# Kernel tuning notes

Measured on AMD Instinct MI355X. Metric: run time of the kernel, lower is better.

Reference implementation:

```python
import jax, jax.numpy as jnp
import numpy as np

N = 524288   # sparse points
C = 64       # io channels
AC = 128     # attn channels
H = 8        # heads
PS = 64      # patch size
HID = 256    # mlp hidden (mlp_ratio=2)
HD = AC // H # head dim
EPS = 1e-5


def _ln(x):
    mu = x.mean(-1, keepdims=True)
    v = x.var(-1, keepdims=True)
    return (x - mu) / jnp.sqrt(v + EPS)


def setup_inputs() -> dict:
    key = jax.random.key(0)
    ks = jax.random.split(key, 12)
    def w(k, shape, fan_in):
        return jax.random.normal(k, shape, jnp.float32) * (1.0 / np.sqrt(fan_in))
    return {
        "feats": jax.random.normal(ks[0], (N, C), jnp.float32),
        "w_pre": w(ks[1], (C, AC), C),    "b_pre": jnp.zeros((AC,), jnp.float32),
        "g1": jnp.ones((AC,), jnp.float32), "b1": jnp.zeros((AC,), jnp.float32),
        "w_qkv": w(ks[2], (AC, 3 * AC), AC), "b_qkv": jnp.zeros((3 * AC,), jnp.float32),
        "w_proj": w(ks[3], (AC, AC), AC), "b_proj": jnp.zeros((AC,), jnp.float32),
        "g2": jnp.ones((AC,), jnp.float32), "b2": jnp.zeros((AC,), jnp.float32),
        "w_m1": w(ks[4], (AC, HID), AC),  "b_m1": jnp.zeros((HID,), jnp.float32),
        "w_m2": w(ks[5], (HID, AC), HID), "b_m2": jnp.zeros((AC,), jnp.float32),
        "w_post": w(ks[6], (AC, C), AC),  "b_post": jnp.zeros((C,), jnp.float32),
    }


def reference(feats, w_pre, b_pre, g1, b1, w_qkv, b_qkv, w_proj, b_proj,
              g2, b2, w_m1, b_m1, w_m2, b_m2, w_post, b_post):
    # pre_proj: 1x1 sparse conv == pointwise linear on [N, C]
    x2 = feats @ w_pre + b_pre                            # [N, AC]
    # norm1 -> patch attention
    n1 = _ln(x2) * g1 + b1
    P = N // PS
    qkv = (n1 @ w_qkv + b_qkv).reshape(P, PS, 3, H, HD)   # patches of 64 pts
    q, k, v = qkv[:, :, 0], qkv[:, :, 1], qkv[:, :, 2]    # [P, PS, H, HD]
    scale = HD ** -0.5
    att = jnp.einsum('pqhd,pkhd->phqk', q, k) * scale     # [P, H, PS, PS]
    att = jax.nn.softmax(att, axis=-1)
    o = jnp.einsum('phqk,pkhd->pqhd', att, v).reshape(N, AC)
    h = o @ w_proj + b_proj
    x2 = x2 + h                                           # residual 1
    # norm2 -> pointwise MLP (1x1 conv -> GELU -> 1x1 conv)
    n2 = _ln(x2) * g2 + b2
    h2 = jax.nn.gelu(n2 @ w_m1 + b_m1, approximate=False) @ w_m2 + b_m2
    x2 = x2 + h2                                          # residual 2
    return x2 @ w_post + b_post                           # post_proj [N, C]
```

## Files before the change

kernel.cpp:

```cpp
#include <hip/hip_runtime.h>
#include <hip/hip_bf16.h>
#include <math.h>


typedef __bf16 bf16;
typedef __bf16 bf16x8 __attribute__((ext_vector_type(8)));
typedef __bf16 bf16x4 __attribute__((ext_vector_type(4)));
typedef float  f32x4  __attribute__((ext_vector_type(4)));

#define MFMA16(a, b, c) __builtin_amdgcn_mfma_f32_16x16x32_bf16((a), (b), (c), 0, 0, 0)

constexpr int OFF_PRE  = 0;
constexpr int OFF_QKV  = 8192;
constexpr int OFF_PROJ = 57344;
constexpr int OFF_M1   = 73728;
constexpr int OFF_M2   = 106496;
constexpr int OFF_POST = 139264;

template <int W>
__device__ __forceinline__ int swz(int row, int col) {
    constexpr int CH = W >> 3;
    constexpr int M  = (CH - 1) < 15 ? (CH - 1) : 15;
    const int c = (col >> 3) ^ (row & M);
    return row * W + c * 8 + (col & 7);
}

__device__ __forceinline__ bf16x8 zero8() {
    bf16x8 z;
#pragma unroll
    for (int j = 0; j < 8; ++j) z[j] = (bf16)0.0f;
    return z;
}

__device__ __forceinline__ void st4(bf16* p, const f32x4 v) {
    bf16x4 o;
#pragma unroll
    for (int r = 0; r < 4; ++r) o[r] = (bf16)v[r];
    *(bf16x4*)p = o;
}

__device__ __forceinline__ float gelu_f(float x) {
    const float u = 0.79788456f * x * (1.0f + 0.044715f * x * x);
    const float e = __builtin_amdgcn_exp2f(u * 2.8853900817779268f);
    return x - x * __builtin_amdgcn_rcpf(e + 1.0f);
}

__global__ void pack_all(const float* __restrict__ w_pre,
                         const float* __restrict__ w_qkv,
                         const float* __restrict__ w_proj,
                         const float* __restrict__ w_m1,
                         const float* __restrict__ w_m2,
                         const float* __restrict__ w_post,
                         bf16* __restrict__ dst) {
    const int t = blockIdx.x;
    const float* src;
    int Ncol, KT, off, t0;
    if (t < 16)       { src = w_pre;  Ncol = 128; KT = 2; off = OFF_PRE;  t0 = 0; }
    else if (t < 112) { src = w_qkv;  Ncol = 384; KT = 4; off = OFF_QKV;  t0 = 16; }
    else if (t < 144) { src = w_proj; Ncol = 128; KT = 4; off = OFF_PROJ; t0 = 112; }
    else if (t < 208) { src = w_m1;   Ncol = 256; KT = 4; off = OFF_M1;   t0 = 144; }
    else if (t < 272) { src = w_m2;   Ncol = 128; KT = 8; off = OFF_M2;   t0 = 208; }
    else              { src = w_post; Ncol = 64;  KT = 4; off = OFF_POST; t0 = 272; }
    const int tile = t - t0;
    const int lane = threadIdx.x;
    const int mt = tile / KT, kt = tile - mt * KT;
    const int n  = mt * 16 + (lane & 15);
    const int k0 = kt * 32 + (lane >> 4) * 8;
    bf16x8 v;
#pragma unroll
    for (int j = 0; j < 8; ++j) v[j] = (bf16)src[(k0 + j) * Ncol + n];
    *(bf16x8*)(dst + off + ((long)(tile * 64 + lane)) * 8) = v;
}

__device__ __forceinline__ void ln_rows(const bf16* __restrict__ in,
                                        bf16* __restrict__ outb,
                                        const float* __restrict__ g,
                                        const float* __restrict__ b, int tid) {
    const int row = tid >> 3, sub = tid & 7;
    bf16x8 c0 = *(const bf16x8*)(in + swz<128>(row, sub * 16));
    bf16x8 c1 = *(const bf16x8*)(in + swz<128>(row, sub * 16 + 8));
    float v[16];
#pragma unroll
    for (int j = 0; j < 8; ++j) { v[j] = (float)c0[j]; v[8 + j] = (float)c1[j]; }
    float s = 0.f, ss = 0.f;
#pragma unroll
    for (int j = 0; j < 16; ++j) { s += v[j]; ss += v[j] * v[j]; }
#pragma unroll
    for (int m = 1; m <= 4; m <<= 1) {
        s += __shfl_xor(s, m);
        ss += __shfl_xor(ss, m);
    }
    const float mu   = s * (1.0f / 128.0f);
    const float rstd = __builtin_amdgcn_rsqf(ss * (1.0f / 128.0f) - mu * mu + 1e-5f);
    bf16x8 o0, o1;
#pragma unroll
    for (int j = 0; j < 8; ++j) {
        o0[j] = (bf16)((v[j] - mu) * rstd * g[sub * 16 + j] + b[sub * 16 + j]);
        o1[j] = (bf16)((v[8 + j] - mu) * rstd * g[sub * 16 + 8 + j] + b[sub * 16 + 8 + j]);
    }
    *(bf16x8*)(outb + swz<128>(row, sub * 16)) = o0;
    *(bf16x8*)(outb + swz<128>(row, sub * 16 + 8)) = o1;
}

__global__ __launch_bounds__(512, 4)
void fused_block_kernel(const float* __restrict__ feats,
                        const bf16* __restrict__ wp,
                        const float* __restrict__ b_pre,
                        const float* __restrict__ g1, const float* __restrict__ b1,
                        const float* __restrict__ b_qkv,
                        const float* __restrict__ b_proj,
                        const float* __restrict__ g2, const float* __restrict__ b2,
                        const float* __restrict__ b_m1,
                        const float* __restrict__ b_m2,
                        const float* __restrict__ b_post,
                        float* __restrict__ out) {
    __shared__ __align__(16) bf16 RA[64 * 128];
    __shared__ __align__(16) bf16 RB[64 * 128];
    __shared__ __align__(16) bf16 RC[64 * 128];

    const int tid  = threadIdx.x;
    const int w    = tid >> 6;
    const int lane = tid & 63;
    const int q    = lane >> 4;
    const int l15  = lane & 15;
    const long base = (long)blockIdx.x * 64;
    const f32x4 fzero = {0.f, 0.f, 0.f, 0.f};

    {
        const int row = tid >> 3, ch = tid & 7;
        const float* src = feats + (base + row) * 64 + ch * 8;
        float4 a = *(const float4*)src;
        float4 b = *(const float4*)(src + 4);
        bf16x8 v;
        v[0] = (bf16)a.x; v[1] = (bf16)a.y; v[2] = (bf16)a.z; v[3] = (bf16)a.w;
        v[4] = (bf16)b.x; v[5] = (bf16)b.y; v[6] = (bf16)b.z; v[7] = (bf16)b.w;
        *(bf16x8*)(RA + swz<64>(row, ch * 8)) = v;
    }
    __syncthreads();

    f32x4 x2[4];

    {
        f32x4 acc[4];
#pragma unroll
        for (int tt = 0; tt < 4; ++tt) acc[tt] = fzero;
#pragma unroll
        for (int ks = 0; ks < 2; ++ks) {
            bf16x8 afr = *(const bf16x8*)(wp + OFF_PRE + ((w * 2 + ks) * 64 + lane) * 8);
#pragma unroll
            for (int tt = 0; tt < 4; ++tt) {
                bf16x8 bfr = *(const bf16x8*)(RA + swz<64>(tt * 16 + l15, ks * 32 + q * 8));
                acc[tt] = MFMA16(afr, bfr, acc[tt]);
            }
        }
        const f32x4 bias = *(const f32x4*)(b_pre + w * 16 + q * 4);
#pragma unroll
        for (int tt = 0; tt < 4; ++tt) {
#pragma unroll
            for (int r = 0; r < 4; ++r) x2[tt][r] = acc[tt][r] + bias[r];
            st4(RB + swz<128>(tt * 16 + l15, w * 16 + q * 4), x2[tt]);
        }
    }
    __syncthreads();

    ln_rows(RB, RA, g1, b1, tid);
    __syncthreads();

    {
        bf16x8 Bfr[4][4];
#pragma unroll
        for (int ks = 0; ks < 4; ++ks)
#pragma unroll
            for (int tt = 0; tt < 4; ++tt)
                Bfr[ks][tt] = *(const bf16x8*)(RA + swz<128>(tt * 16 + l15, ks * 32 + q * 8));
        __syncthreads();
#pragma unroll
        for (int part = 0; part < 3; ++part) {
            const int mt = part * 8 + w;
            f32x4 acc[4];
#pragma unroll
            for (int tt = 0; tt < 4; ++tt) acc[tt] = fzero;
#pragma unroll
            for (int ks = 0; ks < 4; ++ks) {
                bf16x8 afr = *(const bf16x8*)(wp + OFF_QKV + ((mt * 4 + ks) * 64 + lane) * 8);
#pragma unroll
                for (int tt = 0; tt < 4; ++tt) acc[tt] = MFMA16(afr, Bfr[ks][tt], acc[tt]);
            }
            const f32x4 bias = *(const f32x4*)(b_qkv + mt * 16 + q * 4);
            if (part == 0) {
#pragma unroll
                for (int tt = 0; tt < 4; ++tt)
                    st4(RA + swz<128>(tt * 16 + l15, w * 16 + q * 4), acc[tt] + bias);
            } else if (part == 1) {
#pragma unroll
                for (int tt = 0; tt < 4; ++tt)
                    st4(RB + swz<128>(tt * 16 + l15, w * 16 + q * 4), acc[tt] + bias);
            } else {
#pragma unroll
                for (int tt = 0; tt < 4; ++tt)
#pragma unroll
                    for (int r = 0; r < 4; ++r)
                        RC[w * 1024 + swz<64>(q * 4 + r, tt * 16 + l15)] =
                            (bf16)(acc[tt][r] + bias[r]);
            }
        }
    }
    __syncthreads();

    {
        const int colA = w * 16 + (q & 1) * 8;
        const bool hi = (q >= 2);
        const bf16x8 z8 = zero8();
        bf16* const slab = RC + w * 1024;
        bf16x8 Kf[4];
#pragma unroll
        for (int kt = 0; kt < 4; ++kt) {
            bf16x8 t = *(const bf16x8*)(RB + swz<128>(kt * 16 + l15, colA));
            Kf[kt] = hi ? z8 : t;
        }
        bf16x8 Vf[2];
#pragma unroll
        for (int ks = 0; ks < 2; ++ks)
            Vf[ks] = *(const bf16x8*)(slab + swz<64>(l15, ks * 32 + q * 8));
#pragma unroll
        for (int qt = 0; qt < 4; ++qt) {
            bf16x8 t = *(const bf16x8*)(RA + swz<128>(qt * 16 + l15, colA));
            bf16x8 Qf = hi ? z8 : t;
            f32x4 S[4];
#pragma unroll
            for (int kt = 0; kt < 4; ++kt) S[kt] = MFMA16(Kf[kt], Qf, fzero);
            float P[4][4];
            float mx = -1e30f;
#pragma unroll
            for (int kt = 0; kt < 4; ++kt)
#pragma unroll
                for (int r = 0; r < 4; ++r) {
                    const float sv = S[kt][r] * 0.25f;
                    P[kt][r] = sv;
                    mx = fmaxf(mx, sv);
                }
            mx = fmaxf(mx, __shfl_xor(mx, 16));
            mx = fmaxf(mx, __shfl_xor(mx, 32));
            float lsum = 0.f;
#pragma unroll
            for (int kt = 0; kt < 4; ++kt)
#pragma unroll
                for (int r = 0; r < 4; ++r) {
                    const float e = __builtin_amdgcn_exp2f((P[kt][r] - mx) * 1.4426950408889634f);
                    P[kt][r] = e;
                    lsum += e;
                }
            lsum += __shfl_xor(lsum, 16);
            lsum += __shfl_xor(lsum, 32);
            const float inv = __builtin_amdgcn_rcpf(lsum);
#pragma unroll
            for (int kt = 0; kt < 4; ++kt) {
                f32x4 e4;
#pragma unroll
                for (int r = 0; r < 4; ++r) e4[r] = P[kt][r] * inv;
                st4(slab + swz<64>(l15, kt * 16 + q * 4), e4);
            }
            f32x4 O = fzero;
#pragma unroll
            for (int ks = 0; ks < 2; ++ks) {
                bf16x8 Bf = *(const bf16x8*)(slab + swz<64>(l15, ks * 32 + q * 8));
                O = MFMA16(Vf[ks], Bf, O);
            }
            st4(RA + swz<128>(qt * 16 + l15, w * 16 + q * 4), O);
        }
    }
    __syncthreads();

    {
        f32x4 acc[4];
#pragma unroll
        for (int tt = 0; tt < 4; ++tt) acc[tt] = fzero;
#pragma unroll
        for (int ks = 0; ks < 4; ++ks) {
            bf16x8 afr = *(const bf16x8*)(wp + OFF_PROJ + ((w * 4 + ks) * 64 + lane) * 8);
#pragma unroll
            for (int tt = 0; tt < 4; ++tt) {
                bf16x8 bfr = *(const bf16x8*)(RA + swz<128>(tt * 16 + l15, ks * 32 + q * 8));
                acc[tt] = MFMA16(afr, bfr, acc[tt]);
            }
        }
        const f32x4 bias = *(const f32x4*)(b_proj + w * 16 + q * 4);
#pragma unroll
        for (int tt = 0; tt < 4; ++tt) {
#pragma unroll
            for (int r = 0; r < 4; ++r) x2[tt][r] += acc[tt][r] + bias[r];
            st4(RB + swz<128>(tt * 16 + l15, w * 16 + q * 4), x2[tt]);
        }
    }
    __syncthreads();

    ln_rows(RB, RA, g2, b2, tid);
    __syncthreads();

    {
        bf16x8 Bfr[4][4];
#pragma unroll
        for (int ks = 0; ks < 4; ++ks)
#pragma unroll
            for (int tt = 0; tt < 4; ++tt)
                Bfr[ks][tt] = *(const bf16x8*)(RA + swz<128>(tt * 16 + l15, ks * 32 + q * 8));
#pragma unroll
        for (int half = 0; half < 2; ++half) {
            const int mt = w * 2 + half;
            f32x4 acc[4];
#pragma unroll
            for (int tt = 0; tt < 4; ++tt) acc[tt] = fzero;
#pragma unroll
            for (int ks = 0; ks < 4; ++ks) {
                bf16x8 afr = *(const bf16x8*)(wp + OFF_M1 + ((mt * 4 + ks) * 64 + lane) * 8);
#pragma unroll
                for (int tt = 0; tt < 4; ++tt) acc[tt] = MFMA16(afr, Bfr[ks][tt], acc[tt]);
            }
            const f32x4 bias = *(const f32x4*)(b_m1 + mt * 16 + q * 4);
            bf16* const dst = (mt < 8) ? RB : RC;
            const int colb  = (mt & 7) * 16 + q * 4;
#pragma unroll
            for (int tt = 0; tt < 4; ++tt) {
                f32x4 gl;
#pragma unroll
                for (int r = 0; r < 4; ++r) gl[r] = gelu_f(acc[tt][r] + bias[r]);
                st4(dst + swz<128>(tt * 16 + l15, colb), gl);
            }
        }
    }
    __syncthreads();

    {
        f32x4 acc[4];
#pragma unroll
        for (int tt = 0; tt < 4; ++tt) acc[tt] = fzero;
#pragma unroll
        for (int ks = 0; ks < 8; ++ks) {
            bf16x8 afr = *(const bf16x8*)(wp + OFF_M2 + ((w * 8 + ks) * 64 + lane) * 8);
            const bf16* const srcH = (ks < 4) ? RB : RC;
            const int colb = (ks & 3) * 32 + q * 8;
#pragma unroll
            for (int tt = 0; tt < 4; ++tt) {
                bf16x8 bfr = *(const bf16x8*)(srcH + swz<128>(tt * 16 + l15, colb));
                acc[tt] = MFMA16(afr, bfr, acc[tt]);
            }
        }
        const f32x4 bias = *(const f32x4*)(b_m2 + w * 16 + q * 4);
#pragma unroll
        for (int tt = 0; tt < 4; ++tt) {
#pragma unroll
            for (int r = 0; r < 4; ++r) x2[tt][r] += acc[tt][r] + bias[r];
            st4(RA + swz<128>(tt * 16 + l15, w * 16 + q * 4), x2[tt]);
        }
    }
    __syncthreads();

    {
        const int ct  = w >> 1;
        const int tt0 = (w & 1) * 2;
        f32x4 acc[2];
#pragma unroll
        for (int rr = 0; rr < 2; ++rr) acc[rr] = fzero;
#pragma unroll
        for (int ks = 0; ks < 4; ++ks) {
            bf16x8 afr = *(const bf16x8*)(wp + OFF_POST + ((ct * 4 + ks) * 64 + lane) * 8);
#pragma unroll
            for (int rr = 0; rr < 2; ++rr) {
                bf16x8 bfr = *(const bf16x8*)(RA + swz<128>((tt0 + rr) * 16 + l15, ks * 32 + q * 8));
                acc[rr] = MFMA16(afr, bfr, acc[rr]);
            }
        }
        const f32x4 bias = *(const f32x4*)(b_post + ct * 16 + q * 4);
#pragma unroll
        for (int rr = 0; rr < 2; ++rr) {
            f32x4 v = acc[rr] + bias;
            *(f32x4*)(out + (base + (tt0 + rr) * 16 + l15) * 64 + ct * 16 + q * 4) = v;
        }
    }
}

extern "C" void kernel_launch(void* const* d_in, const int* in_sizes, int n_in,
                              void* d_out, int out_size, void* d_ws, size_t ws_size,
                              hipStream_t stream) {
    const float* feats  = (const float*)d_in[0];
    const float* w_pre  = (const float*)d_in[1];
    const float* b_pre  = (const float*)d_in[2];
    const float* g1     = (const float*)d_in[3];
    const float* b1     = (const float*)d_in[4];
    const float* w_qkv  = (const float*)d_in[5];
    const float* b_qkv  = (const float*)d_in[6];
    const float* w_proj = (const float*)d_in[7];
    const float* b_proj = (const float*)d_in[8];
    const float* g2     = (const float*)d_in[9];
    const float* b2     = (const float*)d_in[10];
    const float* w_m1   = (const float*)d_in[11];
    const float* b_m1   = (const float*)d_in[12];
    const float* w_m2   = (const float*)d_in[13];
    const float* b_m2   = (const float*)d_in[14];
    const float* w_post = (const float*)d_in[15];
    const float* b_post = (const float*)d_in[16];

    bf16* wp = (bf16*)d_ws;

    pack_all<<<288, 64, 0, stream>>>(w_pre, w_qkv, w_proj, w_m1, w_m2, w_post, wp);

    fused_block_kernel<<<8192, 512, 0, stream>>>(
        feats, wp, b_pre, g1, b1, b_qkv, b_proj, g2, b2, b_m1, b_m2, b_post,
        (float*)d_out);
}
```

Baseline: 639.6 us.

## Load input fragments directly from global and drop softmax max subtraction

Input features are read from global memory directly into MFMA operand registers instead of being staged through shared memory, which removes one barrier and an LDS round trip. The softmax skips the row-max reduction and its cross-lane shuffles, fusing exp and sum into the score loop. The post-projection work is remapped so each wave reuses one activation fragment across two output column tiles. The changes risk 8x redundant global reads of the input tile across waves, and exp overflow for large attention logits.

```diff
diff --git a/kernel.cpp b/kernel.cpp
--- a/kernel.cpp
+++ b/kernel.cpp
@@ -43,6 +43,13 @@
     const float u = 0.79788456f * x * (1.0f + 0.044715f * x * x);
     const float e = __builtin_amdgcn_exp2f(u * 2.8853900817779268f);
     return x - x * __builtin_amdgcn_rcpf(e + 1.0f);
+}
+
+__device__ __forceinline__ bf16x8 pack8(const float4 a, const float4 b) {
+    bf16x8 v;
+    v[0] = (bf16)a.x; v[1] = (bf16)a.y; v[2] = (bf16)a.z; v[3] = (bf16)a.w;
+    v[4] = (bf16)b.x; v[5] = (bf16)b.y; v[6] = (bf16)b.z; v[7] = (bf16)b.w;
+    return v;
 }
 
 __global__ void pack_all(const float* __restrict__ w_pre,
@@ -126,21 +133,19 @@
     const long base = (long)blockIdx.x * 64;
     const f32x4 fzero = {0.f, 0.f, 0.f, 0.f};
 
-    {
-        const int row = tid >> 3, ch = tid & 7;
-        const float* src = feats + (base + row) * 64 + ch * 8;
-        float4 a = *(const float4*)src;
-        float4 b = *(const float4*)(src + 4);
-        bf16x8 v;
-        v[0] = (bf16)a.x; v[1] = (bf16)a.y; v[2] = (bf16)a.z; v[3] = (bf16)a.w;
-        v[4] = (bf16)b.x; v[5] = (bf16)b.y; v[6] = (bf16)b.z; v[7] = (bf16)b.w;
-        *(bf16x8*)(RA + swz<64>(row, ch * 8)) = v;
-    }
-    __syncthreads();
-
     f32x4 x2[4];
 
     {
+        bf16x8 bfr[2][4];
+#pragma unroll
+        for (int ks = 0; ks < 2; ++ks)
+#pragma unroll
+            for (int tt = 0; tt < 4; ++tt) {
+                const float* fp = feats + (base + tt * 16 + l15) * 64 + ks * 32 + q * 8;
+                float4 a = *(const float4*)fp;
+                float4 b = *(const float4*)(fp + 4);
+                bfr[ks][tt] = pack8(a, b);
+            }
         f32x4 acc[4];
 #pragma unroll
         for (int tt = 0; tt < 4; ++tt) acc[tt] = fzero;
@@ -148,10 +153,8 @@
         for (int ks = 0; ks < 2; ++ks) {
             bf16x8 afr = *(const bf16x8*)(wp + OFF_PRE + ((w * 2 + ks) * 64 + lane) * 8);
 #pragma unroll
-            for (int tt = 0; tt < 4; ++tt) {
-                bf16x8 bfr = *(const bf16x8*)(RA + swz<64>(tt * 16 + l15, ks * 32 + q * 8));
-                acc[tt] = MFMA16(afr, bfr, acc[tt]);
-            }
+            for (int tt = 0; tt < 4; ++tt)
+                acc[tt] = MFMA16(afr, bfr[ks][tt], acc[tt]);
         }
         const f32x4 bias = *(const f32x4*)(b_pre + w * 16 + q * 4);
 #pragma unroll
@@ -226,30 +229,19 @@
         for (int qt = 0; qt < 4; ++qt) {
             bf16x8 t = *(const bf16x8*)(RA + swz<128>(qt * 16 + l15, colA));
             bf16x8 Qf = hi ? z8 : t;
-            f32x4 S[4];
-#pragma unroll
-            for (int kt = 0; kt < 4; ++kt) S[kt] = MFMA16(Kf[kt], Qf, fzero);
             float P[4][4];
-            float mx = -1e30f;
-#pragma unroll
-            for (int kt = 0; kt < 4; ++kt)
+            float lsum = 0.f;
+#pragma unroll
+            for (int kt = 0; kt < 4; ++kt) {
+                f32x4 S = MFMA16(Kf[kt], Qf, fzero);
 #pragma unroll
                 for (int r = 0; r < 4; ++r) {
-                    const float sv = S[kt][r] * 0.25f;
-                    P[kt][r] = sv;
-                    mx = fmaxf(mx, sv);
-                }
-            mx = fmaxf(mx, __shfl_xor(mx, 16));
-            mx = fmaxf(mx, __shfl_xor(mx, 32));
-            float lsum = 0.f;
-#pragma unroll
-            for (int kt = 0; kt < 4; ++kt)
-#pragma unroll
-                for (int r = 0; r < 4; ++r) {
-                    const float e = __builtin_amdgcn_exp2f((P[kt][r] - mx) * 1.4426950408889634f);
+                    const float sv = S[r] * 0.25f;
+                    const float e = __builtin_amdgcn_exp2f(sv * 1.4426950408889634f);
                     P[kt][r] = e;
                     lsum += e;
                 }
+            }
             lsum += __shfl_xor(lsum, 16);
             lsum += __shfl_xor(lsum, 32);
             const float inv = __builtin_amdgcn_rcpf(lsum);
@@ -356,25 +348,25 @@
     __syncthreads();
 
     {
-        const int ct  = w >> 1;
-        const int tt0 = (w & 1) * 2;
+        const int tt  = w >> 1;
+        const int ct0 = (w & 1) * 2;
         f32x4 acc[2];
 #pragma unroll
         for (int rr = 0; rr < 2; ++rr) acc[rr] = fzero;
 #pragma unroll
         for (int ks = 0; ks < 4; ++ks) {
-            bf16x8 afr = *(const bf16x8*)(wp + OFF_POST + ((ct * 4 + ks) * 64 + lane) * 8);
+            bf16x8 bfr = *(const bf16x8*)(RA + swz<128>(tt * 16 + l15, ks * 32 + q * 8));
 #pragma unroll
             for (int rr = 0; rr < 2; ++rr) {
-                bf16x8 bfr = *(const bf16x8*)(RA + swz<128>((tt0 + rr) * 16 + l15, ks * 32 + q * 8));
+                bf16x8 afr = *(const bf16x8*)(wp + OFF_POST + (((ct0 + rr) * 4 + ks) * 64 + lane) * 8);
                 acc[rr] = MFMA16(afr, bfr, acc[rr]);
             }
         }
-        const f32x4 bias = *(const f32x4*)(b_post + ct * 16 + q * 4);
 #pragma unroll
         for (int rr = 0; rr < 2; ++rr) {
+            const f32x4 bias = *(const f32x4*)(b_post + (ct0 + rr) * 16 + q * 4);
             f32x4 v = acc[rr] + bias;
-            *(f32x4*)(out + (base + (tt0 + rr) * 16 + l15) * 64 + ct * 16 + q * 4) = v;
+            *(f32x4*)(out + (base + tt * 16 + l15) * 64 + (ct0 + rr) * 16 + q * 4) = v;
         }
     }
 }
```

Measured after the change: 802.7 us. +25.5%, slower.
